# Optimization experiments

Hardware: AMD Instinct MI355X
Metric: run time of the kernel (lower is better)

The kernel has to match this reference:

```python
import jax, jax.numpy as jnp
import numpy as np

N = 100000        # num nodes
E = 1600000       # num edges (avg degree 16)
D = 64            # in_dim == out_dim (required by x[col] * curvature_weight)


def setup_inputs() -> dict:
    key = jax.random.key(0)
    k1, k2, k3, k4, k5, k6, k7 = jax.random.split(key, 7)
    x = jax.random.normal(k1, (N, D), dtype=jnp.float32)
    edge_index = jax.random.randint(k2, (2, E), 0, N, dtype=jnp.int64)
    curvature = jax.random.normal(k3, (N,), dtype=jnp.float32)
    # nn.Linear(1, D): weight [D, 1], bias [D]
    W_curv = jax.random.normal(k4, (D, 1), dtype=jnp.float32) / jnp.sqrt(1.0)
    b_curv = jax.random.normal(k5, (D,), dtype=jnp.float32) * 0.01
    # nn.Linear(D, D): weight [D, D], bias [D]
    W_lin = jax.random.normal(k6, (D, D), dtype=jnp.float32) / jnp.sqrt(D)
    b_lin = jax.random.normal(k7, (D,), dtype=jnp.float32) * 0.01
    return {"x": x, "curvature": curvature, "W_curv": W_curv, "b_curv": b_curv,
            "W_lin": W_lin, "b_lin": b_lin, "edge_index": edge_index}


def reference(x, curvature, W_curv, b_curv, W_lin, b_lin, edge_index):
    row, col = edge_index[0], edge_index[1]              # [E], [E]
    # |curvature[row] - curvature[col]| -> [E, 1]
    cdiff = jnp.abs(curvature[row] - curvature[col])[:, None]
    # Linear(1, D) + sigmoid gate: [E, D]
    gate = jax.nn.sigmoid(cdiff * W_curv[:, 0] + b_curv)
    # gather source features and gate them: [E, D]
    msg = x[col] * gate
    # scatter_mean by destination node (0 for empty segments, like torch_scatter)
    summed = jax.ops.segment_sum(msg, row, num_segments=N)           # [N, D]
    cnt = jax.ops.segment_sum(jnp.ones((msg.shape[0], 1), msg.dtype), row,
                              num_segments=N)                        # [N, 1]
    mean = summed / jnp.maximum(cnt, 1.0)
    # Linear(D, D) + exact GELU (torch F.gelu default)
    out = jax.nn.gelu(mean @ W_lin.T + b_lin, approximate=False)
    return out
```

## Files before the change

### kernel.cpp

```cpp
#include <hip/hip_runtime.h>
#include <math.h>

#define N_NODES 100000
#define N_EDGES 1600000
#define DIM 64

#define NBUCK 391
#define BCAP  4608
#define TILE  8000

#define NPW 8
#define WPB 4
#define NPB (NPW * WPB)
#define NODE_BLOCKS (N_NODES / NPB)

__device__ __forceinline__ float fast_gate(float s, float wl, float bl2) {
    return __builtin_amdgcn_rcpf(1.0f + __builtin_amdgcn_exp2f(fmaf(s, wl, bl2)));
}

__global__ __launch_bounds__(256) void binA_kernel(
    const int* __restrict__ edge, int* __restrict__ bcnt,
    int* __restrict__ bedge)
{
    __shared__ int hist[NBUCK];
    __shared__ int gbase[NBUCK];
    __shared__ int cur[NBUCK];

    const int t  = threadIdx.x;
    const int e0 = blockIdx.x * TILE;

    for (int i = t; i < NBUCK; i += 256) { hist[i] = 0; cur[i] = 0; }
    __syncthreads();

    for (int i = t; i < TILE; i += 256)
        atomicAdd(&hist[edge[e0 + i] >> 8], 1);
    __syncthreads();

    for (int i = t; i < NBUCK; i += 256) {
        int h = hist[i];
        gbase[i] = (h > 0) ? (i * BCAP + atomicAdd(&bcnt[i], h)) : 0;
    }
    __syncthreads();

    for (int i = t; i < TILE; i += 256) {
        int r = edge[e0 + i];
        int c = edge[N_EDGES + e0 + i];
        int b = r >> 8;
        int lrank = atomicAdd(&cur[b], 1);
        int dst = gbase[b] + lrank;
        if (dst < (b + 1) * BCAP)
            bedge[dst] = ((r & 255) << 17) | c;
    }
}

__global__ __launch_bounds__(256) void binC_kernel(
    const int* __restrict__ bcnt, const int* __restrict__ bedge,
    int* __restrict__ off, int* __restrict__ scol)
{
    __shared__ int red[256];
    __shared__ int lhist[256];
    __shared__ int lscan[256];
    __shared__ int loff[256];
    __shared__ int lcur[256];

    const int t = threadIdx.x;
    const int b = blockIdx.x;

    int ps = 0;
    for (int i = t; i < b; i += 256) ps += bcnt[i];
    red[t] = ps;
    lhist[t] = 0; lcur[t] = 0;
    __syncthreads();
    for (int o = 128; o > 0; o >>= 1) {
        if (t < o) red[t] += red[t + o];
        __syncthreads();
    }
    const int base = red[0];
    const int nb   = min(bcnt[b], BCAP);
    const int src  = b * BCAP;

    for (int j = t; j < nb; j += 256)
        atomicAdd(&lhist[bedge[src + j] >> 17], 1);
    __syncthreads();

    int v = lhist[t];
    lscan[t] = v;
    __syncthreads();
    for (int o = 1; o < 256; o <<= 1) {
        int u = (t >= o) ? lscan[t - o] : 0;
        __syncthreads();
        lscan[t] += u;
        __syncthreads();
    }
    loff[t] = lscan[t] - v;
    __syncthreads();

    const int row = b * 256 + t;
    if (row < N_NODES) off[row] = base + loff[t];
    if (b == 0 && t == 0) off[N_NODES] = N_EDGES;

    for (int j = t; j < nb; j += 256) {
        int pv = bedge[src + j];
        int lr = pv >> 17;
        int rk = atomicAdd(&lcur[lr], 1);
        scol[base + loff[lr] + rk] = pv & 0x1FFFF;
    }
}

__global__ __launch_bounds__(256) void node_kernel(
    const float* __restrict__ x,    const float* __restrict__ curv,
    const int*   __restrict__ off,  const int* __restrict__ scol,
    const float* __restrict__ Wc,   const float* __restrict__ bc,
    const float* __restrict__ Wl,   const float* __restrict__ bl,
    float* __restrict__ out)
{
    __shared__ float Ws[64][65];
    __shared__ float msl[WPB][64];
    __shared__ int2  ecd[WPB][64];

    const int tid = threadIdx.x;
    #pragma unroll
    for (int i = tid; i < DIM * DIM; i += 256)
        Ws[i >> 6][i & 63] = Wl[i];
    __syncthreads();

    const int sub  = tid >> 6;
    const int lane = tid & 63;
    const int eg   = lane >> 4;
    const int fg   = (lane & 15) << 2;
    const int d    = lane;

    const float L2E = 1.44269504088896340736f;
    const float4 wc4 = *(const float4*)&Wc[fg];
    const float4 bc4 = *(const float4*)&bc[fg];
    const float wl0 = -wc4.x * L2E, wl1 = -wc4.y * L2E,
                wl2 = -wc4.z * L2E, wl3 = -wc4.w * L2E;
    const float bq0 = -bc4.x * L2E, bq1 = -bc4.y * L2E,
                bq2 = -bc4.z * L2E, bq3 = -bc4.w * L2E;
    const float bld = bl[d];

    const int nbase = blockIdx.x * NPB + sub * NPW;

    for (int i = 0; i < NPW; ++i) {
        const int   node  = nbase + i;
        const int   start = off[node];
        const int   deg   = off[node + 1] - start;
        const float cn    = curv[node];

        float a0 = 0.f, a1 = 0.f, a2 = 0.f, a3 = 0.f;

        for (int kb = 0; kb < deg; kb += 64) {
            const int pn = min(64, deg - kb);
            if (lane < pn) {
                int   c  = scol[start + kb + lane];
                float cd = fabsf(cn - curv[c]);
                ecd[sub][lane] = make_int2(c, __float_as_int(cd));
            }
            int k = eg;
            for (; k + 4 < pn; k += 8) {
                int2 p0 = ecd[sub][k];
                int2 p1 = ecd[sub][k + 4];
                float s0 = __int_as_float(p0.y);
                float s1 = __int_as_float(p1.y);
                float4 x0 = *(const float4*)&x[((unsigned)p0.x << 6) + fg];
                float4 x1 = *(const float4*)&x[((unsigned)p1.x << 6) + fg];
                a0 = fmaf(x0.x, fast_gate(s0, wl0, bq0), a0);
                a1 = fmaf(x0.y, fast_gate(s0, wl1, bq1), a1);
                a2 = fmaf(x0.z, fast_gate(s0, wl2, bq2), a2);
                a3 = fmaf(x0.w, fast_gate(s0, wl3, bq3), a3);
                a0 = fmaf(x1.x, fast_gate(s1, wl0, bq0), a0);
                a1 = fmaf(x1.y, fast_gate(s1, wl1, bq1), a1);
                a2 = fmaf(x1.z, fast_gate(s1, wl2, bq2), a2);
                a3 = fmaf(x1.w, fast_gate(s1, wl3, bq3), a3);
            }
            if (k < pn) {
                int2 p0 = ecd[sub][k];
                float s0 = __int_as_float(p0.y);
                float4 x0 = *(const float4*)&x[((unsigned)p0.x << 6) + fg];
                a0 = fmaf(x0.x, fast_gate(s0, wl0, bq0), a0);
                a1 = fmaf(x0.y, fast_gate(s0, wl1, bq1), a1);
                a2 = fmaf(x0.z, fast_gate(s0, wl2, bq2), a2);
                a3 = fmaf(x0.w, fast_gate(s0, wl3, bq3), a3);
            }
        }

        a0 += __shfl_xor(a0, 16); a0 += __shfl_xor(a0, 32);
        a1 += __shfl_xor(a1, 16); a1 += __shfl_xor(a1, 32);
        a2 += __shfl_xor(a2, 16); a2 += __shfl_xor(a2, 32);
        a3 += __shfl_xor(a3, 16); a3 += __shfl_xor(a3, 32);

        const float inv = __builtin_amdgcn_rcpf(fmaxf((float)deg, 1.0f));
        if (eg == 0)
            *(float4*)&msl[sub][fg] = make_float4(a0 * inv, a1 * inv, a2 * inv, a3 * inv);

        float r = bld;
        #pragma unroll
        for (int q = 0; q < DIM; q += 4) {
            float4 mv = *(const float4*)&msl[sub][q];
            float4 wv = *(const float4*)&Ws[d][q];
            r = fmaf(mv.x, wv.x, r);
            r = fmaf(mv.y, wv.y, r);
            r = fmaf(mv.z, wv.z, r);
            r = fmaf(mv.w, wv.w, r);
        }
        out[(size_t)node * DIM + d] = 0.5f * r * (1.0f + erff(r * 0.70710678118654752f));
    }
}

extern "C" void kernel_launch(void* const* d_in, const int* in_sizes, int n_in,
                              void* d_out, int out_size, void* d_ws, size_t ws_size,
                              hipStream_t stream) {
    const float* x    = (const float*)d_in[0];
    const float* curv = (const float*)d_in[1];
    const float* Wc   = (const float*)d_in[2];
    const float* bc   = (const float*)d_in[3];
    const float* Wl   = (const float*)d_in[4];
    const float* bl   = (const float*)d_in[5];
    const int*   edge = (const int*)d_in[6];

    float* out = (float*)d_out;

    int* bcnt  = (int*)d_ws;
    int* off   = bcnt + 512;
    int* bedge = off + N_NODES + 1;
    int* scol  = bedge + NBUCK * BCAP;

    hipMemsetAsync(bcnt, 0, 512 * sizeof(int), stream);

    binA_kernel<<<200, 256, 0, stream>>>(edge, bcnt, bedge);
    binC_kernel<<<NBUCK, 256, 0, stream>>>(bcnt, bedge, off, scol);
    node_kernel<<<NODE_BLOCKS, 256, 0, stream>>>(
        x, curv, off, scol, Wc, bc, Wl, bl, out);
}
```

Measured before the change: 150.6 us.

## Fuse per-bucket CSR build into node kernel using shared-memory local sort

Buckets are shrunk to 128 rows. The second binning pass (local histogram, scan and scatter to a global CSR column array) is folded into the node kernel, which sorts its bucket's edges into shared memory and aggregates from there. This removes one kernel launch and the global write and read of the offsets and sorted-column arrays. In exchange, each block uses more LDS and has a serial prologue before aggregation. There are now only 782 large blocks instead of 3125, which may reduce occupancy and load balance.

New measurement: 142.8 us. 5.2% less time.

```diff
diff --git a/kernel.cpp b/kernel.cpp
--- a/kernel.cpp
+++ b/kernel.cpp
@@ -5,14 +5,10 @@
 #define N_EDGES 1600000
 #define DIM 64
 
-#define NBUCK 391
-#define BCAP  4608
+#define RPB   128
+#define NBUCK 782
+#define BCAP  2432
 #define TILE  8000
-
-#define NPW 8
-#define WPB 4
-#define NPB (NPW * WPB)
-#define NODE_BLOCKS (N_NODES / NPB)
 
 __device__ __forceinline__ float fast_gate(float s, float wl, float bl2) {
     return __builtin_amdgcn_rcpf(1.0f + __builtin_amdgcn_exp2f(fmaf(s, wl, bl2)));
@@ -33,7 +29,7 @@
     __syncthreads();
 
     for (int i = t; i < TILE; i += 256)
-        atomicAdd(&hist[edge[e0 + i] >> 8], 1);
+        atomicAdd(&hist[edge[e0 + i] >> 7], 1);
     __syncthreads();
 
     for (int i = t; i < NBUCK; i += 256) {
@@ -45,87 +41,68 @@
     for (int i = t; i < TILE; i += 256) {
         int r = edge[e0 + i];
         int c = edge[N_EDGES + e0 + i];
-        int b = r >> 8;
+        int b = r >> 7;
         int lrank = atomicAdd(&cur[b], 1);
         int dst = gbase[b] + lrank;
         if (dst < (b + 1) * BCAP)
-            bedge[dst] = ((r & 255) << 17) | c;
-    }
-}
-
-__global__ __launch_bounds__(256) void binC_kernel(
-    const int* __restrict__ bcnt, const int* __restrict__ bedge,
-    int* __restrict__ off, int* __restrict__ scol)
-{
-    __shared__ int red[256];
-    __shared__ int lhist[256];
-    __shared__ int lscan[256];
-    __shared__ int loff[256];
-    __shared__ int lcur[256];
-
-    const int t = threadIdx.x;
-    const int b = blockIdx.x;
-
-    int ps = 0;
-    for (int i = t; i < b; i += 256) ps += bcnt[i];
-    red[t] = ps;
-    lhist[t] = 0; lcur[t] = 0;
-    __syncthreads();
-    for (int o = 128; o > 0; o >>= 1) {
-        if (t < o) red[t] += red[t + o];
-        __syncthreads();
-    }
-    const int base = red[0];
-    const int nb   = min(bcnt[b], BCAP);
-    const int src  = b * BCAP;
-
-    for (int j = t; j < nb; j += 256)
-        atomicAdd(&lhist[bedge[src + j] >> 17], 1);
-    __syncthreads();
-
-    int v = lhist[t];
-    lscan[t] = v;
-    __syncthreads();
-    for (int o = 1; o < 256; o <<= 1) {
-        int u = (t >= o) ? lscan[t - o] : 0;
-        __syncthreads();
-        lscan[t] += u;
-        __syncthreads();
-    }
-    loff[t] = lscan[t] - v;
-    __syncthreads();
-
-    const int row = b * 256 + t;
-    if (row < N_NODES) off[row] = base + loff[t];
-    if (b == 0 && t == 0) off[N_NODES] = N_EDGES;
-
-    for (int j = t; j < nb; j += 256) {
-        int pv = bedge[src + j];
-        int lr = pv >> 17;
-        int rk = atomicAdd(&lcur[lr], 1);
-        scol[base + loff[lr] + rk] = pv & 0x1FFFF;
+            bedge[dst] = ((r & 127) << 17) | c;
     }
 }
 
 __global__ __launch_bounds__(256) void node_kernel(
     const float* __restrict__ x,    const float* __restrict__ curv,
-    const int*   __restrict__ off,  const int* __restrict__ scol,
+    const int*   __restrict__ bcnt, const int* __restrict__ bedge,
     const float* __restrict__ Wc,   const float* __restrict__ bc,
     const float* __restrict__ Wl,   const float* __restrict__ bl,
     float* __restrict__ out)
 {
     __shared__ float Ws[64][65];
-    __shared__ float msl[WPB][64];
-    __shared__ int2  ecd[WPB][64];
-
-    const int tid = threadIdx.x;
+    __shared__ float msl[4][64];
+    __shared__ int2  ecd[4][64];
+    __shared__ int   sedge[BCAP];
+    __shared__ int   lhist[RPB];
+    __shared__ int   lscan[RPB];
+    __shared__ int   loff[RPB];
+    __shared__ int   lcur[RPB];
+
+    const int t = threadIdx.x;
+    const int b = blockIdx.x;
+
     #pragma unroll
-    for (int i = tid; i < DIM * DIM; i += 256)
+    for (int i = t; i < DIM * DIM; i += 256)
         Ws[i >> 6][i & 63] = Wl[i];
-    __syncthreads();
-
-    const int sub  = tid >> 6;
-    const int lane = tid & 63;
+    if (t < RPB) { lhist[t] = 0; lcur[t] = 0; }
+    __syncthreads();
+
+    const int nb  = min(bcnt[b], BCAP);
+    const int src = b * BCAP;
+
+    for (int j = t; j < nb; j += 256)
+        atomicAdd(&lhist[bedge[src + j] >> 17], 1);
+    __syncthreads();
+
+    if (t < RPB) lscan[t] = lhist[t];
+    __syncthreads();
+    for (int o = 1; o < RPB; o <<= 1) {
+        int u = 0;
+        if (t < RPB && t >= o) u = lscan[t - o];
+        __syncthreads();
+        if (t < RPB) lscan[t] += u;
+        __syncthreads();
+    }
+    if (t < RPB) loff[t] = lscan[t] - lhist[t];
+    __syncthreads();
+
+    for (int j = t; j < nb; j += 256) {
+        int pv = bedge[src + j];
+        int lr = pv >> 17;
+        int rk = atomicAdd(&lcur[lr], 1);
+        sedge[loff[lr] + rk] = pv & 0x1FFFF;
+    }
+    __syncthreads();
+
+    const int sub  = t >> 6;
+    const int lane = t & 63;
     const int eg   = lane >> 4;
     const int fg   = (lane & 15) << 2;
     const int d    = lane;
@@ -139,12 +116,13 @@
                 bq2 = -bc4.z * L2E, bq3 = -bc4.w * L2E;
     const float bld = bl[d];
 
-    const int nbase = blockIdx.x * NPB + sub * NPW;
-
-    for (int i = 0; i < NPW; ++i) {
-        const int   node  = nbase + i;
-        const int   start = off[node];
-        const int   deg   = off[node + 1] - start;
+    for (int i = 0; i < 32; ++i) {
+        const int lr   = sub * 32 + i;
+        const int node = b * RPB + lr;
+        if (node >= N_NODES) break;
+
+        const int   start = loff[lr];
+        const int   deg   = lhist[lr];
         const float cn    = curv[node];
 
         float a0 = 0.f, a1 = 0.f, a2 = 0.f, a3 = 0.f;
@@ -152,7 +130,7 @@
         for (int kb = 0; kb < deg; kb += 64) {
             const int pn = min(64, deg - kb);
             if (lane < pn) {
-                int   c  = scol[start + kb + lane];
+                int   c  = sedge[start + kb + lane];
                 float cd = fabsf(cn - curv[c]);
                 ecd[sub][lane] = make_int2(c, __float_as_int(cd));
             }
@@ -221,14 +199,11 @@
     float* out = (float*)d_out;
 
     int* bcnt  = (int*)d_ws;
-    int* off   = bcnt + 512;
-    int* bedge = off + N_NODES + 1;
-    int* scol  = bedge + NBUCK * BCAP;
-
-    hipMemsetAsync(bcnt, 0, 512 * sizeof(int), stream);
+    int* bedge = bcnt + 1024;
+
+    hipMemsetAsync(bcnt, 0, 1024 * sizeof(int), stream);
 
     binA_kernel<<<200, 256, 0, stream>>>(edge, bcnt, bedge);
-    binC_kernel<<<NBUCK, 256, 0, stream>>>(bcnt, bedge, off, scol);
-    node_kernel<<<NODE_BLOCKS, 256, 0, stream>>>(
-        x, curv, off, scol, Wc, bc, Wl, bl, out);
-}
+    node_kernel<<<NBUCK, 256, 0, stream>>>(
+        x, curv, bcnt, bedge, Wc, bc, Wl, bl, out);
+}
```
